# Optimization experiments

Measured on AMD Instinct MI355X. Metric: run time of the kernel, lower is better.

The kernel has to match this reference:

```python
import jax, jax.numpy as jnp
import numpy as np

TOP_K = 2
AUX_COEFF = 0.01

def setup_inputs() -> dict:
    key = jax.random.key(0)
    k1, k2, k3, k4 = jax.random.split(key, 4)
    B, T, d, E = 4, 1024, 1024, 8
    x = jax.random.normal(k1, (B, T, d), dtype=jnp.float32)
    w_gate = jax.random.normal(k2, (d, E), dtype=jnp.float32) * 0.02
    w1 = jax.random.normal(k3, (E, d, 4 * d), dtype=jnp.float32) * 0.02
    w2 = jax.random.normal(k4, (E, 4 * d, d), dtype=jnp.float32) * 0.02
    return {"x": x, "w_gate": w_gate, "w1": w1, "w2": w2}

def reference(x, w_gate, w1, w2):
    B, T, d = x.shape
    E = w_gate.shape[1]
    N = B * T
    xf = x.reshape(N, d)

    # Router: softmax over experts, top-k, renormalize
    logits = xf @ w_gate                      # [N, E]
    probs = jax.nn.softmax(logits, axis=-1)   # [N, E]
    topk_p, topk_i = jax.lax.top_k(probs, TOP_K)
    topk_p = topk_p / topk_p.sum(axis=-1, keepdims=True)

    # Combine weights: scatter top-k probs into [N, E] (equiv. to masked scatter-add loop)
    comb = jnp.zeros((N, E), dtype=x.dtype).at[
        jnp.arange(N)[:, None], topk_i].add(topk_p)

    # Grouped expert MLP (dense over experts, weighted combine)
    h = jnp.einsum('nd,edf->enf', xf, w1)     # [E, N, 4d]
    h = jax.nn.gelu(h, approximate=False)     # exact erf GELU like nn.GELU
    y = jnp.einsum('enf,efd->end', h, w2)     # [E, N, d]
    out = jnp.einsum('ne,end->nd', comb, y).reshape(B, T, d)

    # Load-balancing aux loss (training branch)
    counts = jnp.zeros((E,), dtype=x.dtype).at[topk_i.reshape(-1)].add(1.0)
    f = counts / (N * TOP_K)
    p = probs.mean(axis=0)
    aux_loss = AUX_COEFF * E * jnp.sum(f * p)
    return out, aux_loss
```

## Files before the change

### kernel.cpp

```cpp
#include <hip/hip_runtime.h>
#include <cmath>

#define N_TOK 4096
#define DDIM 1024
#define FDIM 4096
#define NEXP 8
#define MAXT 72
#define MAXROWS (MAXT * 128)

typedef __attribute__((ext_vector_type(4))) float f32x4;
typedef __attribute__((ext_vector_type(8))) __bf16 bf16x8;
typedef __attribute__((ext_vector_type(4))) unsigned short us4;
typedef __attribute__((ext_vector_type(8))) unsigned short us8;

__device__ __forceinline__ unsigned short f2bf(float f) {
  unsigned u = __builtin_bit_cast(unsigned, f);
  u += 0x7FFFu + ((u >> 16) & 1u);
  return (unsigned short)(u >> 16);
}

__device__ __forceinline__ void gload16(const void* g, void* l) {
  __builtin_amdgcn_global_load_lds(
      (const __attribute__((address_space(1))) unsigned int*)g,
      (__attribute__((address_space(3))) unsigned int*)l, 16, 0, 0);
}

__device__ __forceinline__ int xcd_remap(int h, int nwg) {
  int q = nwg >> 3, r = nwg & 7;
  int xcd = h & 7, o = h >> 3;
  return (xcd < r ? xcd * (q + 1) : r * (q + 1) + (xcd - r) * q) + o;
}

__global__ __launch_bounds__(64) void router_kernel(
    const float* __restrict__ x, const float* __restrict__ wg,
    float* __restrict__ probs, int* __restrict__ eids, float* __restrict__ ewts,
    unsigned short* __restrict__ xb) {
  int n = blockIdx.x;
  int t = threadIdx.x;
  const float* xr = x + (size_t)n * DDIM;
  f32x4 xv[4];
#pragma unroll
  for (int j = 0; j < 4; j++) xv[j] = *(const f32x4*)(xr + j * 256 + t * 4);
  float acc[8] = {0, 0, 0, 0, 0, 0, 0, 0};
#pragma unroll
  for (int j = 0; j < 4; j++) {
#pragma unroll
    for (int u = 0; u < 4; u++) {
      float v = xv[j][u];
      const float* wr = wg + (size_t)(j * 256 + t * 4 + u) * 8;
#pragma unroll
      for (int e = 0; e < 8; e++) acc[e] = fmaf(v, wr[e], acc[e]);
    }
  }
  unsigned short* xo = xb + (size_t)n * DDIM;
#pragma unroll
  for (int j = 0; j < 4; j++) {
    us4 o = {f2bf(xv[j][0]), f2bf(xv[j][1]), f2bf(xv[j][2]), f2bf(xv[j][3])};
    *(us4*)(xo + j * 256 + t * 4) = o;
  }
#pragma unroll
  for (int off = 32; off > 0; off >>= 1) {
#pragma unroll
    for (int e = 0; e < 8; e++) acc[e] += __shfl_xor(acc[e], off, 64);
  }
  if (t == 0) {
    float mx = acc[0];
#pragma unroll
    for (int e = 1; e < 8; e++) mx = fmaxf(mx, acc[e]);
    float p[8], s = 0.f;
#pragma unroll
    for (int e = 0; e < 8; e++) { p[e] = expf(acc[e] - mx); s += p[e]; }
    float inv = 1.f / s;
#pragma unroll
    for (int e = 0; e < 8; e++) { p[e] *= inv; probs[n * 8 + e] = p[e]; }
    int i0 = 0;
#pragma unroll
    for (int e = 1; e < 8; e++) if (p[e] > p[i0]) i0 = e;
    int i1 = (i0 == 0) ? 1 : 0;
#pragma unroll
    for (int e = 0; e < 8; e++) if (e != i0 && p[e] > p[i1]) i1 = e;
    float sw = p[i0] + p[i1];
    eids[n * 2] = i0; eids[n * 2 + 1] = i1;
    ewts[n * 2] = p[i0] / sw; ewts[n * 2 + 1] = p[i1] / sw;
  }
}

__global__ __launch_bounds__(256) void plan_kernel(
    const float* __restrict__ probs, const int* __restrict__ eids,
    float* __restrict__ aux_out, int* __restrict__ meta) {
  __shared__ float pl[256][8];
  __shared__ int cl[256][8];
  __shared__ float ps2[8];
  __shared__ int cn2[8];
  int t = threadIdx.x;
  float pa[8] = {0, 0, 0, 0, 0, 0, 0, 0};
  int ca[8] = {0, 0, 0, 0, 0, 0, 0, 0};
  for (int n = t; n < N_TOK; n += 256) {
#pragma unroll
    for (int e = 0; e < 8; e++) pa[e] += probs[n * 8 + e];
    ca[eids[n * 2]]++; ca[eids[n * 2 + 1]]++;
  }
#pragma unroll
  for (int e = 0; e < 8; e++) { pl[t][e] = pa[e]; cl[t][e] = ca[e]; }
  __syncthreads();
  if (t < 8) {
    float s = 0; int c = 0;
    for (int i = 0; i < 256; i++) { s += pl[i][t]; c += cl[i][t]; }
    ps2[t] = s; cn2[t] = c;
  }
  __syncthreads();
  if (t == 0) {
    int tb = 0; float aux = 0.f;
    for (int e = 0; e < 8; e++) {
      int c = cn2[e];
      meta[e] = c; meta[8 + e] = 0; meta[16 + e] = tb;
      int tiles = (c + 127) >> 7;
      for (int i = 0; i < tiles; i++) meta[24 + tb + i] = e;
      tb += tiles;
      aux += ((float)c / (float)(N_TOK * 2)) * (ps2[e] / (float)N_TOK);
    }
    meta[96] = tb;
    *aux_out = 0.01f * 8.f * aux;
  }
}

__global__ __launch_bounds__(256) void scatter_kernel(
    const int* __restrict__ eids, int* __restrict__ meta,
    int* __restrict__ perm, int* __restrict__ inv) {
  int n = blockIdx.x * 256 + threadIdx.x;
  if (n >= N_TOK) return;
#pragma unroll
  for (int s = 0; s < 2; s++) {
    int e = eids[n * 2 + s];
    int pos = atomicAdd(&meta[8 + e], 1);
    int row = (meta[16 + e] << 7) + pos;
    perm[row] = n;
    inv[n * 2 + s] = row;
  }
}

__global__ __launch_bounds__(256) void transpose_conv(
    const float* __restrict__ src, unsigned short* __restrict__ dst, int R, int C) {
  __shared__ unsigned short tile[64 * 64];
  size_t eoff = (size_t)blockIdx.z * (size_t)R * (size_t)C;
  src += eoff; dst += eoff;
  int c0 = blockIdx.x << 6, r0 = blockIdx.y << 6;
  int t = threadIdx.x;
  int rl = (t >> 4) << 2;
  int cl = (t & 15) << 2;
  f32x4 v[4];
#pragma unroll
  for (int i = 0; i < 4; i++)
    v[i] = *(const f32x4*)(src + (size_t)(r0 + rl + i) * C + c0 + cl);
#pragma unroll
  for (int u = 0; u < 4; u++) {
    int c = cl + u;
    us4 o = {f2bf(v[0][u]), f2bf(v[1][u]), f2bf(v[2][u]), f2bf(v[3][u])};
    unsigned byteoff = (unsigned)c * 128 + ((((unsigned)(rl >> 3)) ^ (unsigned)(c & 7)) << 4) + (unsigned)(rl & 7) * 2;
    *(us4*)((char*)tile + byteoff) = o;
  }
  __syncthreads();
#pragma unroll
  for (int p = 0; p < 2; p++) {
    int id = t + p * 256;
    int c = id >> 3, q = id & 7;
    unsigned byteoff = (unsigned)c * 128 + (((unsigned)q ^ (unsigned)(c & 7)) << 4);
    us8 val = *(const us8*)((const char*)tile + byteoff);
    *(us8*)(dst + (size_t)(c0 + c) * R + r0 + q * 8) = val;
  }
}

template <int K, int NPANELS, bool GATHER, int MODE>
__global__ __launch_bounds__(256, 2) void gemm_kernel(
    const unsigned short* __restrict__ A,
    const unsigned short* __restrict__ Bt,
    unsigned short* __restrict__ Hout,
    float* __restrict__ Out,
    const int* __restrict__ perm,
    const int* __restrict__ tileExpert, const int* __restrict__ totalTiles,
    int NB) {
  __shared__ unsigned short ldsA[128 * 64];
  __shared__ unsigned short ldsB[128 * 64];
  constexpr int NWG = MAXT * NPANELS;
  int L = xcd_remap((int)blockIdx.x, NWG);
  int sup = L >> 5, wi = L & 31;
  constexpr int GM = MAXT / 8;
  int gm = sup % GM, gn = sup / GM;
  int tile = gm * 8 + (wi & 7);
  int nt = gn * 4 + (wi >> 3);
  if (tile >= *totalTiles) return;
  int e = tileExpert[tile];
  int m0 = tile << 7;
  int n0 = nt << 7;
  const unsigned short* Bbase = Bt + ((size_t)e * NB + n0) * K;
  int t = threadIdx.x;
  int wave = t >> 6, lane = t & 63;
  int g = lane >> 4, ln = lane & 15;
  int wm = wave >> 1, wn = wave & 1;

  const unsigned short* srcA[4];
  const unsigned short* srcB[4];
#pragma unroll
  for (int i = 0; i < 4; i++) {
    int c = wave * 256 + i * 64 + lane;
    int r = c >> 3, kc = c & 7;
    int rowA = GATHER ? perm[m0 + r] : (m0 + r);
    srcA[i] = A + (size_t)rowA * K + ((kc ^ (r & 7)) << 3);
    srcB[i] = Bbase + (size_t)r * K + ((kc ^ (r & 7)) << 3);
  }

  f32x4 acc[4][4];
#pragma unroll
  for (int a = 0; a < 4; a++)
#pragma unroll
    for (int b = 0; b < 4; b++) acc[a][b] = (f32x4){0.f, 0.f, 0.f, 0.f};

  for (int k0 = 0; k0 < K; k0 += 64) {
#pragma unroll
    for (int i = 0; i < 4; i++) {
      int cb = wave * 256 + i * 64;
      gload16(srcA[i] + k0, &ldsA[cb * 8]);
      gload16(srcB[i] + k0, &ldsB[cb * 8]);
    }
    __syncthreads();
#pragma unroll
    for (int ks = 0; ks < 2; ks++) {
      bf16x8 af[4], bfr[4];
      int q = ks * 4 + g;
#pragma unroll
      for (int mf = 0; mf < 4; mf++) {
        int m = wm * 64 + mf * 16 + ln;
        af[mf] = *(const bf16x8*)((const char*)ldsA + m * 128 + ((q ^ (m & 7)) << 4));
      }
#pragma unroll
      for (int nf = 0; nf < 4; nf++) {
        int n = wn * 64 + nf * 16 + ln;
        bfr[nf] = *(const bf16x8*)((const char*)ldsB + n * 128 + ((q ^ (n & 7)) << 4));
      }
#pragma unroll
      for (int mf = 0; mf < 4; mf++)
#pragma unroll
        for (int nf = 0; nf < 4; nf++)
          acc[mf][nf] = __builtin_amdgcn_mfma_f32_16x16x32_bf16(af[mf], bfr[nf], acc[mf][nf], 0, 0, 0);
    }
    __syncthreads();
  }

  if (MODE == 1) {
#pragma unroll
    for (int mf = 0; mf < 4; mf++) {
#pragma unroll
      for (int r = 0; r < 4; r++) {
        int row = m0 + wm * 64 + mf * 16 + g * 4 + r;
        unsigned short* hp = Hout + (size_t)row * NB + n0 + wn * 64 + ln;
#pragma unroll
        for (int nf = 0; nf < 4; nf++) {
          float v = acc[mf][nf][r];
          v = 0.5f * v * (1.f + erff(v * 0.70710678118654752f));
          hp[nf * 16] = f2bf(v);
        }
      }
    }
  } else {
#pragma unroll
    for (int mf = 0; mf < 4; mf++) {
#pragma unroll
      for (int r = 0; r < 4; r++) {
        int row = m0 + wm * 64 + mf * 16 + g * 4 + r;
        float* yp = Out + (size_t)row * NB + n0 + wn * 64 + ln;
#pragma unroll
        for (int nf = 0; nf < 4; nf++) yp[nf * 16] = acc[mf][nf][r];
      }
    }
  }
}

__global__ __launch_bounds__(256) void combine_kernel(
    const float* __restrict__ yscr, const int* __restrict__ inv,
    const float* __restrict__ ewts, float* __restrict__ out) {
  int n = blockIdx.x, t = threadIdx.x;
  int r0 = inv[n * 2], r1 = inv[n * 2 + 1];
  float w0 = ewts[n * 2], w1 = ewts[n * 2 + 1];
  f32x4 a = *(const f32x4*)(yscr + (size_t)r0 * DDIM + t * 4);
  f32x4 b = *(const f32x4*)(yscr + (size_t)r1 * DDIM + t * 4);
  f32x4 o;
#pragma unroll
  for (int j = 0; j < 4; j++) o[j] = w0 * a[j] + w1 * b[j];
  *(f32x4*)(out + (size_t)n * DDIM + t * 4) = o;
}

extern "C" void kernel_launch(void* const* d_in, const int* in_sizes, int n_in,
                              void* d_out, int out_size, void* d_ws, size_t ws_size,
                              hipStream_t stream) {
  const float* x = (const float*)d_in[0];
  const float* wgate = (const float*)d_in[1];
  const float* w1 = (const float*)d_in[2];
  const float* w2 = (const float*)d_in[3];
  float* out = (float*)d_out;

  char* w = (char*)d_ws;
  float* probs = (float*)w;                 w += (size_t)N_TOK * 8 * 4;
  int* eids = (int*)w;                      w += (size_t)N_TOK * 2 * 4;
  float* ewts = (float*)w;                  w += (size_t)N_TOK * 2 * 4;
  int* meta = (int*)w;                      w += 512;
  int* perm = (int*)w;                      w += (size_t)MAXROWS * 4;
  int* inv = (int*)w;                       w += (size_t)N_TOK * 2 * 4;
  unsigned short* xb = (unsigned short*)w;  w += (size_t)N_TOK * DDIM * 2;
  unsigned short* w1t = (unsigned short*)w; w += (size_t)NEXP * DDIM * FDIM * 2;
  unsigned short* w2t = (unsigned short*)w; w += (size_t)NEXP * DDIM * FDIM * 2;
  unsigned short* h = (unsigned short*)w;   w += (size_t)MAXROWS * FDIM * 2;
  float* yscr = (float*)w1t;

  hipMemsetAsync(perm, 0, (size_t)MAXROWS * 4, stream);

  router_kernel<<<N_TOK, 64, 0, stream>>>(x, wgate, probs, eids, ewts, xb);
  plan_kernel<<<1, 256, 0, stream>>>(probs, eids, out + 4194304, meta);
  scatter_kernel<<<16, 256, 0, stream>>>(eids, meta, perm, inv);
  transpose_conv<<<dim3(64, 16, 8), 256, 0, stream>>>(w1, w1t, DDIM, FDIM);
  transpose_conv<<<dim3(16, 64, 8), 256, 0, stream>>>(w2, w2t, FDIM, DDIM);
  gemm_kernel<DDIM, 32, true, 1><<<MAXT * 32, 256, 0, stream>>>(
      xb, w1t, h, nullptr, perm, meta + 24, meta + 96, FDIM);
  gemm_kernel<FDIM, 8, false, 2><<<MAXT * 8, 256, 0, stream>>>(
      h, w2t, nullptr, yscr, perm, meta + 24, meta + 96, DDIM);
  combine_kernel<<<N_TOK, 256, 0, stream>>>(yscr, inv, ewts, out);
}
```

Before: 388.6 us.

## Double-buffer LDS tiles in expert GEMM to overlap loads with MFMA

Replaces the single-buffered K loop, which had two barriers per step, with a ping-pong pair of LDS buffers for A and B. Each step reads its fragments from the current buffer, then issues the async global-to-LDS loads for the next K slice before running the MFMAs, leaving one barrier per step. This is meant to hide global load latency behind compute. It doubles LDS use to 64KB per block, which can cut occupancy below the declared two blocks per CU, and it keeps both half-K fragment sets live in registers.

```diff
diff --git a/kernel.cpp b/kernel.cpp
--- a/kernel.cpp
+++ b/kernel.cpp
@@ -170,6 +170,47 @@
   }
 }
 
+
+#define STAGE_DB(NA, NB_, ko)                                                  \
+  _Pragma("unroll") for (int i = 0; i < 4; i++) {                              \
+    gload16(srcA[i] + (ko), (char*)(NA) + ldsoff[i]);                          \
+    gload16(srcB[i] + (ko), (char*)(NB_) + ldsoff[i]);                         \
+  }
+
+#define FRAGS_DB(CA, CB)                                                       \
+  bf16x8 af0[4], bf0[4], af1[4], bf1[4];                                       \
+  _Pragma("unroll") for (int mf = 0; mf < 4; mf++) {                           \
+    int m = wm * 64 + mf * 16 + ln;                                            \
+    af0[mf] = *(const bf16x8*)((const char*)(CA) + m * 128 + ((g ^ (m & 7)) << 4));         \
+    af1[mf] = *(const bf16x8*)((const char*)(CA) + m * 128 + (((4 + g) ^ (m & 7)) << 4));   \
+  }                                                                            \
+  _Pragma("unroll") for (int nf = 0; nf < 4; nf++) {                           \
+    int nn = wn * 64 + nf * 16 + ln;                                           \
+    bf0[nf] = *(const bf16x8*)((const char*)(CB) + nn * 128 + ((g ^ (nn & 7)) << 4));       \
+    bf1[nf] = *(const bf16x8*)((const char*)(CB) + nn * 128 + (((4 + g) ^ (nn & 7)) << 4)); \
+  }
+
+#define MFMAS_DB                                                               \
+  _Pragma("unroll") for (int mf = 0; mf < 4; mf++)                             \
+  _Pragma("unroll") for (int nf = 0; nf < 4; nf++) {                           \
+    acc[mf][nf] = __builtin_amdgcn_mfma_f32_16x16x32_bf16(af0[mf], bf0[nf], acc[mf][nf], 0, 0, 0); \
+    acc[mf][nf] = __builtin_amdgcn_mfma_f32_16x16x32_bf16(af1[mf], bf1[nf], acc[mf][nf], 0, 0, 0); \
+  }
+
+#define BODY_DB(CA, CB, NA, NB_, ko)                                           \
+  {                                                                            \
+    FRAGS_DB(CA, CB)                                                           \
+    STAGE_DB(NA, NB_, ko)                                                      \
+    MFMAS_DB                                                                   \
+    __syncthreads();                                                           \
+  }
+
+#define BODY_LAST(CA, CB)                                                      \
+  {                                                                            \
+    FRAGS_DB(CA, CB)                                                           \
+    MFMAS_DB                                                                   \
+  }
+
 template <int K, int NPANELS, bool GATHER, int MODE>
 __global__ __launch_bounds__(256, 2) void gemm_kernel(
     const unsigned short* __restrict__ A,
@@ -179,8 +220,13 @@
     const int* __restrict__ perm,
     const int* __restrict__ tileExpert, const int* __restrict__ totalTiles,
     int NB) {
-  __shared__ unsigned short ldsA[128 * 64];
-  __shared__ unsigned short ldsB[128 * 64];
+  constexpr int NT = K / 64;
+  static_assert(NT % 2 == 0, "NT even");
+  __shared__ unsigned short ldsA0[8192];
+  __shared__ unsigned short ldsB0[8192];
+  __shared__ unsigned short ldsA1[8192];
+  __shared__ unsigned short ldsB1[8192];
+
   constexpr int NWG = MAXT * NPANELS;
   int L = xcd_remap((int)blockIdx.x, NWG);
   int sup = L >> 5, wi = L & 31;
@@ -200,6 +246,7 @@
 
   const unsigned short* srcA[4];
   const unsigned short* srcB[4];
+  unsigned ldsoff[4];
 #pragma unroll
   for (int i = 0; i < 4; i++) {
     int c = wave * 256 + i * 64 + lane;
@@ -207,6 +254,7 @@
     int rowA = GATHER ? perm[m0 + r] : (m0 + r);
     srcA[i] = A + (size_t)rowA * K + ((kc ^ (r & 7)) << 3);
     srcB[i] = Bbase + (size_t)r * K + ((kc ^ (r & 7)) << 3);
+    ldsoff[i] = (unsigned)(wave * 256 + i * 64) * 16u;
   }
 
   f32x4 acc[4][4];
@@ -215,36 +263,15 @@
 #pragma unroll
     for (int b = 0; b < 4; b++) acc[a][b] = (f32x4){0.f, 0.f, 0.f, 0.f};
 
-  for (int k0 = 0; k0 < K; k0 += 64) {
-#pragma unroll
-    for (int i = 0; i < 4; i++) {
-      int cb = wave * 256 + i * 64;
-      gload16(srcA[i] + k0, &ldsA[cb * 8]);
-      gload16(srcB[i] + k0, &ldsB[cb * 8]);
-    }
-    __syncthreads();
-#pragma unroll
-    for (int ks = 0; ks < 2; ks++) {
-      bf16x8 af[4], bfr[4];
-      int q = ks * 4 + g;
-#pragma unroll
-      for (int mf = 0; mf < 4; mf++) {
-        int m = wm * 64 + mf * 16 + ln;
-        af[mf] = *(const bf16x8*)((const char*)ldsA + m * 128 + ((q ^ (m & 7)) << 4));
-      }
-#pragma unroll
-      for (int nf = 0; nf < 4; nf++) {
-        int n = wn * 64 + nf * 16 + ln;
-        bfr[nf] = *(const bf16x8*)((const char*)ldsB + n * 128 + ((q ^ (n & 7)) << 4));
-      }
-#pragma unroll
-      for (int mf = 0; mf < 4; mf++)
-#pragma unroll
-        for (int nf = 0; nf < 4; nf++)
-          acc[mf][nf] = __builtin_amdgcn_mfma_f32_16x16x32_bf16(af[mf], bfr[nf], acc[mf][nf], 0, 0, 0);
-    }
-    __syncthreads();
-  }
+  STAGE_DB(ldsA0, ldsB0, 0)
+  __syncthreads();
+
+  for (int p = 0; p < NT / 2 - 1; ++p) {
+    BODY_DB(ldsA0, ldsB0, ldsA1, ldsB1, (2 * p + 1) * 64)
+    BODY_DB(ldsA1, ldsB1, ldsA0, ldsB0, (2 * p + 2) * 64)
+  }
+  BODY_DB(ldsA0, ldsB0, ldsA1, ldsB1, (NT - 1) * 64)
+  BODY_LAST(ldsA1, ldsB1)
 
   if (MODE == 1) {
 #pragma unroll
```

Result: slower. 443.0 us (+14.0%).
